# Performance work log

Hardware: AMD Instinct MI355X
Metric: run time of the kernel (lower is better)

Reference implementation:

```python
import jax, jax.numpy as jnp
import numpy as np

VOCAB = 30523      # 30522 regular tokens + span-marker token id 30522
SPAN_TOK = 30522
D = 768
N_DOCS = 64
N_PASS = 1024
TITLE_LEN = 128
SEQ = 256
N_EDGES = 32768
N_NODES = N_DOCS + 2 * N_PASS   # docs || passages || spans (one span per passage)
N_REL = 2
TAU = 0.2


def setup_inputs() -> dict:
    key = jax.random.key(0)
    ks = jax.random.split(key, 12)
    doc_ids = jax.random.randint(ks[0], (N_DOCS, TITLE_LEN), 0, SPAN_TOK, dtype=jnp.int32)
    pass_ids = jax.random.randint(ks[1], (N_PASS, SEQ), 0, SPAN_TOK, dtype=jnp.int32)
    # place exactly one span-marker token per passage at a random non-CLS position
    pos = jax.random.randint(ks[2], (N_PASS,), 1, SEQ, dtype=jnp.int32)
    pass_ids = pass_ids.at[jnp.arange(N_PASS), pos].set(SPAN_TOK)
    edge_index = jax.random.randint(ks[3], (2, N_EDGES), 0, N_NODES, dtype=jnp.int32)
    edge_type = jax.random.randint(ks[4], (N_EDGES,), 0, N_REL, dtype=jnp.int32)
    s = 0.02
    return {
        "document_title_input_ids": doc_ids,
        "passages_input_ids": pass_ids,
        "edge_index": edge_index,
        "edge_type": edge_type,
        "embed": jax.random.normal(ks[5], (VOCAB, D), jnp.float32) * s,
        "w_root1": jax.random.normal(ks[6], (D, D), jnp.float32) * s,
        "w_rel1": jax.random.normal(ks[7], (N_REL, D, D), jnp.float32) * s,
        "b1": jnp.zeros((D,), jnp.float32),
        "w_root2": jax.random.normal(ks[8], (D, D), jnp.float32) * s,
        "w_rel2": jax.random.normal(ks[9], (N_REL, D, D), jnp.float32) * s,
        "b2": jnp.zeros((D,), jnp.float32),
        "clf_w": jax.random.normal(ks[10], (D, 1), jnp.float32) * s,
        "clf_b": jnp.zeros((1,), jnp.float32),
    }


def _rgcn(x, src, dst, edge_type, w_root, w_rel, b):
    # PyG RGCNConv: out_i = x_i W_root + b + sum_r mean_{j in N_r(i)} x_j W_r
    out = x @ w_root + b
    xs = x[src]  # [E, D] gather
    for r in range(N_REL):
        w = (edge_type == r).astype(x.dtype)[:, None]  # [E,1]
        num = jax.ops.segment_sum(xs * w, dst, num_segments=N_NODES)  # [N, D]
        cnt = jax.ops.segment_sum(w, dst, num_segments=N_NODES)       # [N, 1]
        out = out + (num / jnp.maximum(cnt, 1.0)) @ w_rel[r]
    return out


def reference(document_title_input_ids, passages_input_ids, edge_index, edge_type,
              embed, w_root1, w_rel1, b1, w_root2, w_rel2, b2, clf_w, clf_b):
    # encoder (pretrained BERT stand-in): token embedding lookup -> last_hidden_state
    title_feat = embed[document_title_input_ids][:, 0, :]   # [N_DOCS, D]  CLS
    pass_emb = embed[passages_input_ids]                     # [N_PASS, SEQ, D]
    pass_feat = pass_emb[:, 0, :]                            # [N_PASS, D]  CLS
    # span-token gather: torch.where(ids == 30522) -> one marker per passage
    rows, cols = jnp.nonzero(passages_input_ids == SPAN_TOK, size=N_PASS)
    span_feat = pass_emb[rows, cols]                         # [N_PASS, D]
    x = jnp.concatenate((title_feat, pass_feat, span_feat), axis=0)  # [N_NODES, D]
    src, dst = edge_index[0], edge_index[1]
    x = _rgcn(x, src, dst, edge_type, w_root1, w_rel1, b1)
    x = _rgcn(x, src, dst, edge_type, w_root2, w_rel2, b2)
    scores = jax.nn.sigmoid(x @ clf_w + clf_b).reshape(-1)   # [N_NODES]
    span_score = jnp.exp(scores[-N_PASS:] / TAU)             # [N_PASS]
    return span_score
```

## Files before the change

### kernel.cpp

```cpp
#include <hip/hip_runtime.h>

#define NDOCS 64
#define NPASS 1024
#define TITLE_LEN 128
#define SEQ 256
#define NEDGES 32768
#define NNODES 2112
#define DIM 768
#define SPAN_TOK 30522
#define NREL 2
#define NBINS (NREL * NNODES)
#define SPAN0 (NNODES - NPASS)
#define CLRWORDS (NNODES * 6 + NPASS * 2 + NBINS)

__device__ inline float wred(float s) {
#pragma unroll
  for (int off = 32; off > 0; off >>= 1) s += __shfl_down(s, off);
  return s;
}
__device__ inline float dot4(float4 a, float4 b) {
  return a.x * b.x + a.y * b.y + a.z * b.z + a.w * b.w;
}

__global__ __launch_bounds__(256) void foldv_kernel(
    const float* __restrict__ w_root2, const float* __restrict__ w_rel2,
    const float* __restrict__ b2, const float* __restrict__ clf_w,
    const float* __restrict__ clf_b, float* __restrict__ v,
    int* __restrict__ clrbase) {
  int b = blockIdx.x;
  if (b < 577) {
    int k = b * 4 + (threadIdx.x >> 6);
    int lane = threadIdx.x & 63;
    if (k > 3 * DIM) return;
    const float* row = (k < DIM) ? w_root2 + (size_t)k * DIM
                     : (k < 3 * DIM) ? w_rel2 + (size_t)(k - DIM) * DIM
                                     : b2;
    const float4* r4 = (const float4*)row;
    const float4* w4 = (const float4*)clf_w;
    float s = 0.f;
#pragma unroll
    for (int i = 0; i < 3; ++i) {
      int j = lane + i * 64;
      s += dot4(r4[j], w4[j]);
    }
    s = wred(s);
    if (lane == 0) v[k] = s + (k == 3 * DIM ? clf_b[0] : 0.f);
  } else {
    int i = (b - 577) * 256 + threadIdx.x;
    if (i < CLRWORDS) clrbase[i] = 0;
  }
}

__global__ __launch_bounds__(256) void foldu_hist_kernel(
    const float* __restrict__ w_root1, const float* __restrict__ w_rel1,
    const float* __restrict__ b1, const float* __restrict__ v,
    float4* __restrict__ U4, const int* __restrict__ dst,
    const int* __restrict__ et, int* __restrict__ deg) {
  int b = blockIdx.x;
  if (b < 577) {
    int k = b * 4 + (threadIdx.x >> 6);
    int lane = threadIdx.x & 63;
    if (k > 3 * DIM) return;
    const float* row = (k < DIM) ? w_root1 + (size_t)k * DIM
                     : (k < 3 * DIM) ? w_rel1 + (size_t)(k - DIM) * DIM
                                     : b1;
    const float4* r4 = (const float4*)row;
    const float4* v0 = (const float4*)v;
    const float4* v1 = (const float4*)(v + DIM);
    const float4* v2 = (const float4*)(v + 2 * DIM);
    float s0 = 0.f, s1 = 0.f, s2 = 0.f;
#pragma unroll
    for (int i = 0; i < 3; ++i) {
      int j = lane + i * 64;
      float4 r = r4[j];
      s0 += dot4(r, v0[j]);
      s1 += dot4(r, v1[j]);
      s2 += dot4(r, v2[j]);
    }
    s0 = wred(s0); s1 = wred(s1); s2 = wred(s2);
    if (lane == 0) U4[k] = make_float4(s0, s1, s2, 0.f);
  } else {
    int e = (b - 577) * 256 + threadIdx.x;
    atomicAdd(&deg[et[e] * NNODES + dst[e]], 1);
  }
}

__global__ __launch_bounds__(256) void t_kernel(
    const int* __restrict__ doc_ids, const int* __restrict__ pass_ids,
    const float* __restrict__ embed, const float4* __restrict__ U4,
    float4* __restrict__ Tq) {
  int m = blockIdx.x * 4 + (threadIdx.x >> 6);
  int lane = threadIdx.x & 63;
  int tok = (m < NDOCS) ? doc_ids[m * TITLE_LEN]
          : (m < NDOCS + NPASS) ? pass_ids[(m - NDOCS) * SEQ]
                                : SPAN_TOK;
  const float4* e4 = (const float4*)(embed + (size_t)tok * DIM);
  float s[9] = {};
#pragma unroll
  for (int i = 0; i < 3; ++i) {
    int j = lane + i * 64;
    float4 ev = e4[j];
#pragma unroll
    for (int q = 0; q < 4; ++q) {
      int k = j * 4 + q;
      float e1 = (q == 0) ? ev.x : (q == 1) ? ev.y : (q == 2) ? ev.z : ev.w;
      float4 u0 = U4[k], u1 = U4[DIM + k], u2 = U4[2 * DIM + k];
      s[0] += e1 * u0.x; s[1] += e1 * u0.y; s[2] += e1 * u0.z;
      s[3] += e1 * u1.x; s[4] += e1 * u1.y; s[5] += e1 * u1.z;
      s[6] += e1 * u2.x; s[7] += e1 * u2.y; s[8] += e1 * u2.z;
    }
  }
#pragma unroll
  for (int a = 0; a < 9; ++a) s[a] = wred(s[a]);
  if (lane == 0) {
    Tq[m * 4 + 0] = make_float4(s[0], s[1], s[2], 0.f);
    Tq[m * 4 + 1] = make_float4(s[3], s[4], s[5], 0.f);
    Tq[m * 4 + 2] = make_float4(s[6], s[7], s[8], 0.f);
  }
}

__global__ __launch_bounds__(256) void pacc_kernel(
    const int* __restrict__ src, const int* __restrict__ dst,
    const int* __restrict__ et, const float4* __restrict__ Tq,
    float* __restrict__ accP) {
  int e = blockIdx.x * 256 + threadIdx.x;
  int s = src[e], d = dst[e], r = et[e];
  float4 t = Tq[s * 4 + 1 + r];
  atomicAdd(&accP[d * 6 + 0 + r], t.x);
  atomicAdd(&accP[d * 6 + 2 + r], t.y);
  atomicAdd(&accP[d * 6 + 4 + r], t.z);
}

__global__ __launch_bounds__(256) void zacc_kernel(
    const int* __restrict__ src, const int* __restrict__ dst,
    const int* __restrict__ et, const float4* __restrict__ Tq,
    const float* __restrict__ accP, const int* __restrict__ deg,
    const float4* __restrict__ U4, float* __restrict__ zacc) {
  int e = blockIdx.x * 256 + threadIdx.x;
  int d = dst[e];
  if (d < SPAN0) return;
  int s = src[e], r = et[e];
  int j = 1 + r;
  float i0 = 1.f / fmaxf((float)deg[s], 1.f);
  float i1 = 1.f / fmaxf((float)deg[NNODES + s], 1.f);
  float t0j = ((const float*)(Tq + (size_t)s * 4))[j];
  float a0 = accP[s * 6 + j * 2 + 0];
  float a1 = accP[s * 6 + j * 2 + 1];
  float dj = ((const float*)(U4 + 3 * DIM))[j];
  float P = t0j + a0 * i0 + a1 * i1 + dj;
  atomicAdd(&zacc[(d - SPAN0) * 2 + r], P);
}

__global__ __launch_bounds__(256) void final_kernel(
    const float4* __restrict__ Tq, const float* __restrict__ accP,
    const int* __restrict__ deg, const float* __restrict__ zacc,
    const float4* __restrict__ U4, const float* __restrict__ v,
    float* __restrict__ out) {
  int i = blockIdx.x * 256 + threadIdx.x;
  if (i >= NPASS) return;
  int n = SPAN0 + i;
  float i0 = 1.f / fmaxf((float)deg[n], 1.f);
  float i1 = 1.f / fmaxf((float)deg[NNODES + n], 1.f);
  float P0 = Tq[n * 4].x + accP[n * 6 + 0] * i0 + accP[n * 6 + 1] * i1 +
             U4[3 * DIM].x;
  float z = P0 + zacc[i * 2 + 0] * i0 + zacc[i * 2 + 1] * i1 + v[3 * DIM];
  float sc = 1.f / (1.f + expf(-z));
  out[i] = expf(sc * 5.f);
}

extern "C" void kernel_launch(void* const* d_in, const int* in_sizes, int n_in,
                              void* d_out, int out_size, void* d_ws, size_t ws_size,
                              hipStream_t stream) {
  const int* doc_ids = (const int*)d_in[0];
  const int* pass_ids = (const int*)d_in[1];
  const int* edge_index = (const int*)d_in[2];
  const int* etype = (const int*)d_in[3];
  const float* embed = (const float*)d_in[4];
  const float* w_root1 = (const float*)d_in[5];
  const float* w_rel1 = (const float*)d_in[6];
  const float* b1 = (const float*)d_in[7];
  const float* w_root2 = (const float*)d_in[8];
  const float* w_rel2 = (const float*)d_in[9];
  const float* b2 = (const float*)d_in[10];
  const float* clf_w = (const float*)d_in[11];
  const float* clf_b = (const float*)d_in[12];
  float* out = (float*)d_out;

  const int* src = edge_index;
  const int* dst = edge_index + NEDGES;

  float4* U4 = (float4*)d_ws;
  float4* Tq = U4 + (3 * DIM + 1);
  float* v = (float*)(Tq + (size_t)NNODES * 4);
  float* accP = v + (3 * DIM + 1);
  float* zacc = accP + NNODES * 6;
  int* deg = (int*)(zacc + NPASS * 2);

  foldv_kernel<<<577 + 74, 256, 0, stream>>>(w_root2, w_rel2, b2, clf_w, clf_b,
                                             v, (int*)accP);
  foldu_hist_kernel<<<577 + 128, 256, 0, stream>>>(w_root1, w_rel1, b1, v, U4,
                                                   dst, etype, deg);
  t_kernel<<<NNODES / 4, 256, 0, stream>>>(doc_ids, pass_ids, embed, U4, Tq);
  pacc_kernel<<<NEDGES / 256, 256, 0, stream>>>(src, dst, etype, Tq, accP);
  zacc_kernel<<<NEDGES / 256, 256, 0, stream>>>(src, dst, etype, Tq, accP, deg,
                                                U4, zacc);
  final_kernel<<<NPASS / 256, 256, 0, stream>>>(Tq, accP, deg, zacc, U4, v, out);
}
```

Measured before the change: 37.50 us.

## Replace zacc atomic pass with CSR bucketing and per-span wave gather

Builds a CSR layout of edges by (relation, destination) using a prefix scan over the degree histogram and an atomic scatter into a permutation array. The final kernel then gathers each span node's incoming edges with one wave per node, instead of running a separate atomic zacc pass over all edges. The scan and scatter are fused into the existing t and pacc launches, so the pipeline drops from six kernels to five. In exchange it adds a serial single-block scan, an atomic scatter, and irregular per-lane gathers in the final kernel.

```diff
diff --git a/kernel.cpp b/kernel.cpp
--- a/kernel.cpp
+++ b/kernel.cpp
@@ -11,7 +11,7 @@
 #define NREL 2
 #define NBINS (NREL * NNODES)
 #define SPAN0 (NNODES - NPASS)
-#define CLRWORDS (NNODES * 6 + NPASS * 2 + NBINS)
+#define CLRWORDS (NNODES * 6 + NBINS)
 
 __device__ inline float wred(float s) {
 #pragma unroll
@@ -22,7 +22,7 @@
   return a.x * b.x + a.y * b.y + a.z * b.z + a.w * b.w;
 }
 
-__global__ __launch_bounds__(256) void foldv_kernel(
+__global__ __launch_bounds__(256) void foldv_clear_kernel(
     const float* __restrict__ w_root2, const float* __restrict__ w_rel2,
     const float* __restrict__ b2, const float* __restrict__ clf_w,
     const float* __restrict__ clf_b, float* __restrict__ v,
@@ -47,18 +47,21 @@
     if (lane == 0) v[k] = s + (k == 3 * DIM ? clf_b[0] : 0.f);
   } else {
     int i = (b - 577) * 256 + threadIdx.x;
-    if (i < CLRWORDS) clrbase[i] = 0;
-  }
-}
-
-__global__ __launch_bounds__(256) void foldu_hist_kernel(
-    const float* __restrict__ w_root1, const float* __restrict__ w_rel1,
-    const float* __restrict__ b1, const float* __restrict__ v,
-    float4* __restrict__ U4, const int* __restrict__ dst,
-    const int* __restrict__ et, int* __restrict__ deg) {
-  int b = blockIdx.x;
-  if (b < 577) {
-    int k = b * 4 + (threadIdx.x >> 6);
+    clrbase[i] = 0;
+  }
+}
+
+__global__ __launch_bounds__(256) void hist_foldu_kernel(
+    const int* __restrict__ dst, const int* __restrict__ et,
+    int* __restrict__ deg, const float* __restrict__ w_root1,
+    const float* __restrict__ w_rel1, const float* __restrict__ b1,
+    const float* __restrict__ v, float4* __restrict__ U4) {
+  int b = blockIdx.x;
+  if (b < 128) {
+    int e = b * 256 + threadIdx.x;
+    atomicAdd(&deg[et[e] * NNODES + dst[e]], 1);
+  } else {
+    int k = (b - 128) * 4 + (threadIdx.x >> 6);
     int lane = threadIdx.x & 63;
     if (k > 3 * DIM) return;
     const float* row = (k < DIM) ? w_root1 + (size_t)k * DIM
@@ -79,93 +82,134 @@
     }
     s0 = wred(s0); s1 = wred(s1); s2 = wred(s2);
     if (lane == 0) U4[k] = make_float4(s0, s1, s2, 0.f);
-  } else {
-    int e = (b - 577) * 256 + threadIdx.x;
-    atomicAdd(&deg[et[e] * NNODES + dst[e]], 1);
-  }
-}
-
-__global__ __launch_bounds__(256) void t_kernel(
+  }
+}
+
+__global__ __launch_bounds__(256) void t_scan_kernel(
     const int* __restrict__ doc_ids, const int* __restrict__ pass_ids,
     const float* __restrict__ embed, const float4* __restrict__ U4,
-    float4* __restrict__ Tq) {
-  int m = blockIdx.x * 4 + (threadIdx.x >> 6);
-  int lane = threadIdx.x & 63;
-  int tok = (m < NDOCS) ? doc_ids[m * TITLE_LEN]
-          : (m < NDOCS + NPASS) ? pass_ids[(m - NDOCS) * SEQ]
-                                : SPAN_TOK;
-  const float4* e4 = (const float4*)(embed + (size_t)tok * DIM);
-  float s[9] = {};
-#pragma unroll
-  for (int i = 0; i < 3; ++i) {
-    int j = lane + i * 64;
-    float4 ev = e4[j];
-#pragma unroll
-    for (int q = 0; q < 4; ++q) {
-      int k = j * 4 + q;
-      float e1 = (q == 0) ? ev.x : (q == 1) ? ev.y : (q == 2) ? ev.z : ev.w;
-      float4 u0 = U4[k], u1 = U4[DIM + k], u2 = U4[2 * DIM + k];
-      s[0] += e1 * u0.x; s[1] += e1 * u0.y; s[2] += e1 * u0.z;
-      s[3] += e1 * u1.x; s[4] += e1 * u1.y; s[5] += e1 * u1.z;
-      s[6] += e1 * u2.x; s[7] += e1 * u2.y; s[8] += e1 * u2.z;
-    }
-  }
-#pragma unroll
-  for (int a = 0; a < 9; ++a) s[a] = wred(s[a]);
-  if (lane == 0) {
-    Tq[m * 4 + 0] = make_float4(s[0], s[1], s[2], 0.f);
-    Tq[m * 4 + 1] = make_float4(s[3], s[4], s[5], 0.f);
-    Tq[m * 4 + 2] = make_float4(s[6], s[7], s[8], 0.f);
-  }
-}
-
-__global__ __launch_bounds__(256) void pacc_kernel(
-    const int* __restrict__ src, const int* __restrict__ dst,
-    const int* __restrict__ et, const float4* __restrict__ Tq,
-    float* __restrict__ accP) {
-  int e = blockIdx.x * 256 + threadIdx.x;
-  int s = src[e], d = dst[e], r = et[e];
-  float4 t = Tq[s * 4 + 1 + r];
-  atomicAdd(&accP[d * 6 + 0 + r], t.x);
-  atomicAdd(&accP[d * 6 + 2 + r], t.y);
-  atomicAdd(&accP[d * 6 + 4 + r], t.z);
-}
-
-__global__ __launch_bounds__(256) void zacc_kernel(
-    const int* __restrict__ src, const int* __restrict__ dst,
-    const int* __restrict__ et, const float4* __restrict__ Tq,
-    const float* __restrict__ accP, const int* __restrict__ deg,
-    const float4* __restrict__ U4, float* __restrict__ zacc) {
-  int e = blockIdx.x * 256 + threadIdx.x;
-  int d = dst[e];
-  if (d < SPAN0) return;
-  int s = src[e], r = et[e];
-  int j = 1 + r;
-  float i0 = 1.f / fmaxf((float)deg[s], 1.f);
-  float i1 = 1.f / fmaxf((float)deg[NNODES + s], 1.f);
-  float t0j = ((const float*)(Tq + (size_t)s * 4))[j];
-  float a0 = accP[s * 6 + j * 2 + 0];
-  float a1 = accP[s * 6 + j * 2 + 1];
-  float dj = ((const float*)(U4 + 3 * DIM))[j];
-  float P = t0j + a0 * i0 + a1 * i1 + dj;
-  atomicAdd(&zacc[(d - SPAN0) * 2 + r], P);
+    float4* __restrict__ Tq, const int* __restrict__ deg,
+    int* __restrict__ offs, int* __restrict__ cur) {
+  __shared__ int part[256];
+  int b = blockIdx.x;
+  int tid = threadIdx.x;
+  if (b < 528) {
+    int m = b * 4 + (tid >> 6);
+    int lane = tid & 63;
+    int tok = (m < NDOCS) ? doc_ids[m * TITLE_LEN]
+            : (m < NDOCS + NPASS) ? pass_ids[(m - NDOCS) * SEQ]
+                                  : SPAN_TOK;
+    const float4* e4 = (const float4*)(embed + (size_t)tok * DIM);
+    float s[9] = {};
+#pragma unroll
+    for (int i = 0; i < 3; ++i) {
+      int j = lane + i * 64;
+      float4 ev = e4[j];
+#pragma unroll
+      for (int q = 0; q < 4; ++q) {
+        int k = j * 4 + q;
+        float e1 = (q == 0) ? ev.x : (q == 1) ? ev.y : (q == 2) ? ev.z : ev.w;
+        float4 u0 = U4[k], u1 = U4[DIM + k], u2 = U4[2 * DIM + k];
+        s[0] += e1 * u0.x; s[1] += e1 * u0.y; s[2] += e1 * u0.z;
+        s[3] += e1 * u1.x; s[4] += e1 * u1.y; s[5] += e1 * u1.z;
+        s[6] += e1 * u2.x; s[7] += e1 * u2.y; s[8] += e1 * u2.z;
+      }
+    }
+#pragma unroll
+    for (int a = 0; a < 9; ++a) s[a] = wred(s[a]);
+    if (lane == 0) {
+      Tq[m * 4 + 0] = make_float4(s[0], s[1], s[2], 0.f);
+      Tq[m * 4 + 1] = make_float4(s[3], s[4], s[5], 0.f);
+      Tq[m * 4 + 2] = make_float4(s[6], s[7], s[8], 0.f);
+    }
+  } else {
+    int loc[17];
+    int s = 0;
+#pragma unroll
+    for (int i = 0; i < 17; ++i) {
+      int idx = tid * 17 + i;
+      loc[i] = s;
+      s += (idx < NBINS) ? deg[idx] : 0;
+    }
+    part[tid] = s;
+    __syncthreads();
+    for (int off = 1; off < 256; off <<= 1) {
+      int val = (tid >= off) ? part[tid - off] : 0;
+      __syncthreads();
+      part[tid] += val;
+      __syncthreads();
+    }
+    int pre = (tid == 0) ? 0 : part[tid - 1];
+#pragma unroll
+    for (int i = 0; i < 17; ++i) {
+      int idx = tid * 17 + i;
+      if (idx <= NBINS) {
+        int val = pre + loc[i];
+        offs[idx] = val;
+        if (idx < NBINS) cur[idx] = val;
+      }
+    }
+  }
+}
+
+__global__ __launch_bounds__(256) void scatter_pacc_kernel(
+    const int* __restrict__ srcv, const int* __restrict__ dst,
+    const int* __restrict__ et, int* __restrict__ cur, int* __restrict__ perm,
+    const float4* __restrict__ Tq, float* __restrict__ accP) {
+  int b = blockIdx.x;
+  if (b < 128) {
+    int e = b * 256 + threadIdx.x;
+    int bin = et[e] * NNODES + dst[e];
+    int p = atomicAdd(&cur[bin], 1);
+    perm[p] = srcv[e];
+  } else {
+    int e = (b - 128) * 256 + threadIdx.x;
+    int s = srcv[e], d = dst[e], r = et[e];
+    float4 t = Tq[s * 4 + 1 + r];
+    atomicAdd(&accP[d * 6 + 0 + r], t.x);
+    atomicAdd(&accP[d * 6 + 2 + r], t.y);
+    atomicAdd(&accP[d * 6 + 4 + r], t.z);
+  }
 }
 
 __global__ __launch_bounds__(256) void final_kernel(
     const float4* __restrict__ Tq, const float* __restrict__ accP,
-    const int* __restrict__ deg, const float* __restrict__ zacc,
+    const int* __restrict__ offs, const int* __restrict__ perm,
     const float4* __restrict__ U4, const float* __restrict__ v,
     float* __restrict__ out) {
-  int i = blockIdx.x * 256 + threadIdx.x;
-  if (i >= NPASS) return;
+  int i = blockIdx.x * 4 + (threadIdx.x >> 6);
+  int lane = threadIdx.x & 63;
   int n = SPAN0 + i;
-  float i0 = 1.f / fmaxf((float)deg[n], 1.f);
-  float i1 = 1.f / fmaxf((float)deg[NNODES + n], 1.f);
-  float P0 = Tq[n * 4].x + accP[n * 6 + 0] * i0 + accP[n * 6 + 1] * i1 +
-             U4[3 * DIM].x;
-  float z = P0 + zacc[i * 2 + 0] * i0 + zacc[i * 2 + 1] * i1 + v[3 * DIM];
-  float sc = 1.f / (1.f + expf(-z));
-  out[i] = expf(sc * 5.f);
+  float4 D = U4[3 * DIM];
+  float zterm = 0.f;
+#pragma unroll
+  for (int r = 0; r < NREL; ++r) {
+    int bin = r * NNODES + n;
+    int beg = offs[bin], end = offs[bin + 1];
+    int cnt = end - beg;
+    if (cnt <= 0) continue;
+    int j = 1 + r;
+    float psum = 0.f;
+    for (int e = beg + lane; e < end; e += 64) {
+      int s = perm[e];
+      float i0 = 1.f / fmaxf((float)(offs[s + 1] - offs[s]), 1.f);
+      float i1 = 1.f / fmaxf((float)(offs[NNODES + s + 1] - offs[NNODES + s]), 1.f);
+      const float* t0 = (const float*)(Tq + (size_t)s * 4);
+      float Ps = t0[j] + accP[s * 6 + j * 2 + 0] * i0 +
+                 accP[s * 6 + j * 2 + 1] * i1 + ((const float*)&D)[j];
+      psum += Ps;
+    }
+    zterm += psum / (float)cnt;
+  }
+  zterm = wred(zterm);
+  if (lane == 0) {
+    float i0 = 1.f / fmaxf((float)(offs[n + 1] - offs[n]), 1.f);
+    float i1 = 1.f / fmaxf((float)(offs[NNODES + n + 1] - offs[NNODES + n]), 1.f);
+    float P0 = Tq[n * 4].x + accP[n * 6 + 0] * i0 + accP[n * 6 + 1] * i1 + D.x;
+    float z = P0 + zterm + v[3 * DIM];
+    float sc = 1.f / (1.f + expf(-z));
+    out[i] = expf(sc * 5.f);
+  }
 }
 
 extern "C" void kernel_launch(void* const* d_in, const int* in_sizes, int n_in,
@@ -193,16 +237,18 @@
   float4* Tq = U4 + (3 * DIM + 1);
   float* v = (float*)(Tq + (size_t)NNODES * 4);
   float* accP = v + (3 * DIM + 1);
-  float* zacc = accP + NNODES * 6;
-  int* deg = (int*)(zacc + NPASS * 2);
-
-  foldv_kernel<<<577 + 74, 256, 0, stream>>>(w_root2, w_rel2, b2, clf_w, clf_b,
-                                             v, (int*)accP);
-  foldu_hist_kernel<<<577 + 128, 256, 0, stream>>>(w_root1, w_rel1, b1, v, U4,
-                                                   dst, etype, deg);
-  t_kernel<<<NNODES / 4, 256, 0, stream>>>(doc_ids, pass_ids, embed, U4, Tq);
-  pacc_kernel<<<NEDGES / 256, 256, 0, stream>>>(src, dst, etype, Tq, accP);
-  zacc_kernel<<<NEDGES / 256, 256, 0, stream>>>(src, dst, etype, Tq, accP, deg,
-                                                U4, zacc);
-  final_kernel<<<NPASS / 256, 256, 0, stream>>>(Tq, accP, deg, zacc, U4, v, out);
-}
+  int* deg = (int*)(accP + NNODES * 6);
+  int* offs = deg + NBINS;
+  int* cur = offs + NBINS + 1;
+  int* perm = cur + NBINS;
+
+  foldv_clear_kernel<<<577 + 66, 256, 0, stream>>>(w_root2, w_rel2, b2, clf_w,
+                                                   clf_b, v, (int*)accP);
+  hist_foldu_kernel<<<128 + 577, 256, 0, stream>>>(dst, etype, deg, w_root1,
+                                                   w_rel1, b1, v, U4);
+  t_scan_kernel<<<528 + 1, 256, 0, stream>>>(doc_ids, pass_ids, embed, U4, Tq,
+                                             deg, offs, cur);
+  scatter_pacc_kernel<<<128 + 128, 256, 0, stream>>>(src, dst, etype, cur, perm,
+                                                     Tq, accP);
+  final_kernel<<<NPASS / 4, 256, 0, stream>>>(Tq, accP, offs, perm, U4, v, out);
+}
```

After: 39.07 us. +4.2%, slower.

## Replace atomic edge scatter kernels with per-node source buckets and gather-based final pass

Applied to the files above, without the earlier changes.

Builds fixed-capacity per-(relation, destination) source lists during the degree histogram. This replaces the float atomic scatter kernels for node partials and span accumulators with a gather in the final kernel, one wavefront per span node, walking two-hop neighbourhoods. It cuts two launches and most float atomics, and it computes Tq only for distinct non-span rows. The trade-off is redundant two-hop work per span node, and edges are silently dropped if any bin exceeds 48 entries.

```diff
diff --git a/kernel.cpp b/kernel.cpp
--- a/kernel.cpp
+++ b/kernel.cpp
@@ -11,7 +11,7 @@
 #define NREL 2
 #define NBINS (NREL * NNODES)
 #define SPAN0 (NNODES - NPASS)
-#define CLRWORDS (NNODES * 6 + NPASS * 2 + NBINS)
+#define CAP 48
 
 __device__ inline float wred(float s) {
 #pragma unroll
@@ -22,11 +22,11 @@
   return a.x * b.x + a.y * b.y + a.z * b.z + a.w * b.w;
 }
 
-__global__ __launch_bounds__(256) void foldv_kernel(
+__global__ __launch_bounds__(256) void foldv_clear_kernel(
     const float* __restrict__ w_root2, const float* __restrict__ w_rel2,
     const float* __restrict__ b2, const float* __restrict__ clf_w,
     const float* __restrict__ clf_b, float* __restrict__ v,
-    int* __restrict__ clrbase) {
+    int* __restrict__ deg) {
   int b = blockIdx.x;
   if (b < 577) {
     int k = b * 4 + (threadIdx.x >> 6);
@@ -47,18 +47,24 @@
     if (lane == 0) v[k] = s + (k == 3 * DIM ? clf_b[0] : 0.f);
   } else {
     int i = (b - 577) * 256 + threadIdx.x;
-    if (i < CLRWORDS) clrbase[i] = 0;
-  }
-}
-
-__global__ __launch_bounds__(256) void foldu_hist_kernel(
+    if (i < NBINS) deg[i] = 0;
+  }
+}
+
+__global__ __launch_bounds__(256) void bucket_foldu_kernel(
+    const int* __restrict__ srcv, const int* __restrict__ dst,
+    const int* __restrict__ et, int* __restrict__ deg, int* __restrict__ bucket,
     const float* __restrict__ w_root1, const float* __restrict__ w_rel1,
     const float* __restrict__ b1, const float* __restrict__ v,
-    float4* __restrict__ U4, const int* __restrict__ dst,
-    const int* __restrict__ et, int* __restrict__ deg) {
+    float4* __restrict__ U4) {
   int b = blockIdx.x;
-  if (b < 577) {
-    int k = b * 4 + (threadIdx.x >> 6);
+  if (b < 128) {
+    int e = b * 256 + threadIdx.x;
+    int bin = et[e] * NNODES + dst[e];
+    int slot = atomicAdd(&deg[bin], 1);
+    if (slot < CAP) bucket[bin * CAP + slot] = srcv[e];
+  } else {
+    int k = (b - 128) * 4 + (threadIdx.x >> 6);
     int lane = threadIdx.x & 63;
     if (k > 3 * DIM) return;
     const float* row = (k < DIM) ? w_root1 + (size_t)k * DIM
@@ -79,9 +85,6 @@
     }
     s0 = wred(s0); s1 = wred(s1); s2 = wred(s2);
     if (lane == 0) U4[k] = make_float4(s0, s1, s2, 0.f);
-  } else {
-    int e = (b - 577) * 256 + threadIdx.x;
-    atomicAdd(&deg[et[e] * NNODES + dst[e]], 1);
   }
 }
 
@@ -91,6 +94,7 @@
     float4* __restrict__ Tq) {
   int m = blockIdx.x * 4 + (threadIdx.x >> 6);
   int lane = threadIdx.x & 63;
+  if (m > SPAN0) return;
   int tok = (m < NDOCS) ? doc_ids[m * TITLE_LEN]
           : (m < NDOCS + NPASS) ? pass_ids[(m - NDOCS) * SEQ]
                                 : SPAN_TOK;
@@ -119,53 +123,49 @@
   }
 }
 
-__global__ __launch_bounds__(256) void pacc_kernel(
-    const int* __restrict__ src, const int* __restrict__ dst,
-    const int* __restrict__ et, const float4* __restrict__ Tq,
-    float* __restrict__ accP) {
-  int e = blockIdx.x * 256 + threadIdx.x;
-  int s = src[e], d = dst[e], r = et[e];
-  float4 t = Tq[s * 4 + 1 + r];
-  atomicAdd(&accP[d * 6 + 0 + r], t.x);
-  atomicAdd(&accP[d * 6 + 2 + r], t.y);
-  atomicAdd(&accP[d * 6 + 4 + r], t.z);
-}
-
-__global__ __launch_bounds__(256) void zacc_kernel(
-    const int* __restrict__ src, const int* __restrict__ dst,
-    const int* __restrict__ et, const float4* __restrict__ Tq,
-    const float* __restrict__ accP, const int* __restrict__ deg,
-    const float4* __restrict__ U4, float* __restrict__ zacc) {
-  int e = blockIdx.x * 256 + threadIdx.x;
-  int d = dst[e];
-  if (d < SPAN0) return;
-  int s = src[e], r = et[e];
-  int j = 1 + r;
-  float i0 = 1.f / fmaxf((float)deg[s], 1.f);
-  float i1 = 1.f / fmaxf((float)deg[NNODES + s], 1.f);
-  float t0j = ((const float*)(Tq + (size_t)s * 4))[j];
-  float a0 = accP[s * 6 + j * 2 + 0];
-  float a1 = accP[s * 6 + j * 2 + 1];
-  float dj = ((const float*)(U4 + 3 * DIM))[j];
-  float P = t0j + a0 * i0 + a1 * i1 + dj;
-  atomicAdd(&zacc[(d - SPAN0) * 2 + r], P);
-}
-
 __global__ __launch_bounds__(256) void final_kernel(
-    const float4* __restrict__ Tq, const float* __restrict__ accP,
-    const int* __restrict__ deg, const float* __restrict__ zacc,
-    const float4* __restrict__ U4, const float* __restrict__ v,
-    float* __restrict__ out) {
-  int i = blockIdx.x * 256 + threadIdx.x;
-  if (i >= NPASS) return;
+    const float4* __restrict__ Tq, const int* __restrict__ deg,
+    const int* __restrict__ bucket, const float4* __restrict__ U4,
+    const float* __restrict__ v, float* __restrict__ out) {
+  int i = blockIdx.x * 4 + (threadIdx.x >> 6);
+  int lane = threadIdx.x & 63;
   int n = SPAN0 + i;
-  float i0 = 1.f / fmaxf((float)deg[n], 1.f);
-  float i1 = 1.f / fmaxf((float)deg[NNODES + n], 1.f);
-  float P0 = Tq[n * 4].x + accP[n * 6 + 0] * i0 + accP[n * 6 + 1] * i1 +
-             U4[3 * DIM].x;
-  float z = P0 + zacc[i * 2 + 0] * i0 + zacc[i * 2 + 1] * i1 + v[3 * DIM];
-  float sc = 1.f / (1.f + expf(-z));
-  out[i] = expf(sc * 5.f);
+  const float* Tqf = (const float*)Tq;
+  float4 D = U4[3 * DIM];
+  const float* Df = (const float*)&D;
+  int c0n = deg[n], c1n = deg[NNODES + n];
+  float i0n = 1.f / fmaxf((float)c0n, 1.f);
+  float i1n = 1.f / fmaxf((float)c1n, 1.f);
+  int tot = c0n + c1n;
+  float zpart = 0.f;
+  for (int o = lane; o < tot; o += 64) {
+    int r = (o < c0n) ? 0 : 1;
+    int oo = (o < c0n) ? o : o - c0n;
+    int s = bucket[(r * NNODES + n) * CAP + oo];
+    int j = 1 + r;
+    int ts = (s < SPAN0) ? s : SPAN0;
+    float inner = Tqf[ts * 16 + j * 4 + 0]
+                + Tqf[ts * 16 + j]
+                + Df[j];
+#pragma unroll
+    for (int rp = 0; rp < 2; ++rp) {
+      int cs = deg[rp * NNODES + s];
+      float ssum = 0.f;
+      for (int e = 0; e < cs; ++e) {
+        int sp = bucket[(rp * NNODES + s) * CAP + e];
+        int tsp = (sp < SPAN0) ? sp : SPAN0;
+        ssum += Tqf[tsp * 16 + (1 + rp) * 4 + j];
+      }
+      inner += ssum / fmaxf((float)cs, 1.f);
+    }
+    zpart += ((r == 0) ? i0n : i1n) * inner;
+  }
+  zpart = wred(zpart);
+  if (lane == 0) {
+    float z = Tqf[SPAN0 * 16 + 0] + Df[0] + v[3 * DIM] + zpart;
+    float sc = 1.f / (1.f + expf(-z));
+    out[i] = expf(sc * 5.f);
+  }
 }
 
 extern "C" void kernel_launch(void* const* d_in, const int* in_sizes, int n_in,
@@ -191,18 +191,15 @@
 
   float4* U4 = (float4*)d_ws;
   float4* Tq = U4 + (3 * DIM + 1);
-  float* v = (float*)(Tq + (size_t)NNODES * 4);
-  float* accP = v + (3 * DIM + 1);
-  float* zacc = accP + NNODES * 6;
-  int* deg = (int*)(zacc + NPASS * 2);
-
-  foldv_kernel<<<577 + 74, 256, 0, stream>>>(w_root2, w_rel2, b2, clf_w, clf_b,
-                                             v, (int*)accP);
-  foldu_hist_kernel<<<577 + 128, 256, 0, stream>>>(w_root1, w_rel1, b1, v, U4,
-                                                   dst, etype, deg);
-  t_kernel<<<NNODES / 4, 256, 0, stream>>>(doc_ids, pass_ids, embed, U4, Tq);
-  pacc_kernel<<<NEDGES / 256, 256, 0, stream>>>(src, dst, etype, Tq, accP);
-  zacc_kernel<<<NEDGES / 256, 256, 0, stream>>>(src, dst, etype, Tq, accP, deg,
-                                                U4, zacc);
-  final_kernel<<<NPASS / 256, 256, 0, stream>>>(Tq, accP, deg, zacc, U4, v, out);
-}
+  float* v = (float*)(Tq + (size_t)(SPAN0 + 1) * 4);
+  int* deg = (int*)(v + 3 * DIM + 1);
+  int* bucket = deg + NBINS;
+
+  foldv_clear_kernel<<<577 + 17, 256, 0, stream>>>(w_root2, w_rel2, b2, clf_w,
+                                                   clf_b, v, deg);
+  bucket_foldu_kernel<<<128 + 577, 256, 0, stream>>>(src, dst, etype, deg,
+                                                     bucket, w_root1, w_rel1,
+                                                     b1, v, U4);
+  t_kernel<<<273, 256, 0, stream>>>(doc_ids, pass_ids, embed, U4, Tq);
+  final_kernel<<<NPASS / 4, 256, 0, stream>>>(Tq, deg, bucket, U4, v, out);
+}
```

Result: faster. 34.93 us (-6.9%).
